# Performance work log

Hardware: AMD Instinct MI355X
Metric: run time of the kernel (lower is better)

The kernel has to match this reference:

```python
import jax, jax.numpy as jnp
import numpy as np

L, M, K, N = 131072, 511, 512, 512
STRIDE = (L - N) // (M - 1)  # 256; stride*(M-1)+N == L
B = 128
KH = K // 2 + 1  # 257 one-sided bins


def _tukey(n_pts, alpha=0.25):
    # scipy.signal.windows.tukey, sym=True
    n = np.arange(n_pts, dtype=np.float64)
    edge = alpha * (n_pts - 1) / 2.0
    w = np.ones(n_pts)
    left = n < edge
    w[left] = 0.5 * (1.0 + np.cos(np.pi * (2.0 * n[left] / (alpha * (n_pts - 1)) - 1.0)))
    right = n > (n_pts - 1) - edge
    w[right] = 0.5 * (1.0 + np.cos(np.pi * (2.0 * n[right] / (alpha * (n_pts - 1)) - 2.0 / alpha + 1.0)))
    return w


def _make_consts():
    w = _tukey(N, 0.25)
    w = (w / w.sum()).astype(np.float32)
    # fourier_matrix[n, k] = exp(-2*pi*i/N)**(n*k), sliced to K//2+1 cols, * sqrt(N)
    nk = np.outer(np.arange(N, dtype=np.float64), np.arange(K, dtype=np.float64))
    sigma = np.exp(-2j * np.pi / N)
    fm = (sigma ** nk)[:, :KH] * np.sqrt(N)
    return jnp.asarray(w), jnp.asarray(fm.astype(np.complex64))


def setup_inputs() -> dict:
    key = jax.random.key(0)
    x = jax.random.normal(key, (B, L), dtype=jnp.float32)
    window, fourier_matrix = _make_consts()
    return {"x": x, "window": window, "fourier_matrix": fourier_matrix}


def reference(x, window, fourier_matrix):
    xc = x.astype(jnp.complex64)
    xc = xc - jnp.mean(xc, axis=1, keepdims=True)
    # unfold(1, N, STRIDE) -> [B, M, N] overlapping frames
    idx = jnp.arange(M)[:, None] * STRIDE + jnp.arange(N)[None, :]  # [M, N]
    frames = xc[:, idx] * window[None, None, :].astype(jnp.complex64)  # [B, M, N]
    spec = jnp.matmul(frames, fourier_matrix)  # [B, M, KH] complex
    return jnp.abs(spec)
```

## Files before the change

kernel.cpp:

```cpp
#include <hip/hip_runtime.h>
#include <math.h>

#define L_LEN    131072
#define M_FRAMES 511
#define N_FFT    512
#define KH       257
#define FSTRIDE  256
#define B_BATCH  128

#define TM       32
#define RSTRIDE  36
#define SQRT_N   22.62741699796952f

typedef float pkf2 __attribute__((ext_vector_type(2)));

__device__ __forceinline__ pkf2 pk_fma(pkf2 a, pkf2 b, pkf2 c) {
    pkf2 d; asm("v_pk_fma_f32 %0, %1, %2, %3" : "=v"(d) : "v"(a), "v"(b), "v"(c)); return d;
}
__device__ __forceinline__ pkf2 pk_mul(pkf2 a, pkf2 b) {
    pkf2 d; asm("v_pk_mul_f32 %0, %1, %2" : "=v"(d) : "v"(a), "v"(b)); return d;
}
__device__ __forceinline__ float hw_sin_rev(float rev){float r;asm("v_sin_f32 %0, %1":"=v"(r):"v"(rev));return r;}
__device__ __forceinline__ float hw_cos_rev(float rev){float r;asm("v_cos_f32 %0, %1":"=v"(r):"v"(rev));return r;}

__global__ __launch_bounds__(256) void pmean_kernel(const float* __restrict__ x,
                                                    float* __restrict__ partial) {
    const int b = blockIdx.x >> 3, chunk = blockIdx.x & 7;
    const float4* p = (const float4*)(x + (size_t)b * L_LEN + (size_t)chunk * (L_LEN / 8));
    float s = 0.f;
    const int nvec = L_LEN / 8 / 4;
    for (int i = threadIdx.x; i < nvec; i += 256) {
        float4 v = p[i];
        s += (v.x + v.y) + (v.z + v.w);
    }
    for (int off = 32; off; off >>= 1) s += __shfl_down(s, off, 64);
    __shared__ float ws[4];
    if ((threadIdx.x & 63) == 0) ws[threadIdx.x >> 6] = s;
    __syncthreads();
    if (threadIdx.x == 0) partial[blockIdx.x] = (ws[0] + ws[1]) + (ws[2] + ws[3]);
}

__global__ __launch_bounds__(256, 2) void spec_kernel(const float* __restrict__ x,
                                                      const float* __restrict__ w,
                                                      const float* __restrict__ partial,
                                                      float* __restrict__ out) {
    __shared__ __align__(16) float lds[256 * RSTRIDE * 2 + 512 + 256];
    float* Es  = lds;
    float* Os  = lds + 256 * RSTRIDE;
    float* wl  = lds + 512 * RSTRIDE;
    float* nyq = wl + 512;

    const int b  = blockIdx.x;
    const int m0 = blockIdx.y * TM;
    const int t  = threadIdx.x;

    float msum = 0.f;
    #pragma unroll
    for (int i = 0; i < 8; ++i) msum += partial[(b << 3) + i];
    const float mean = msum * (1.0f / (float)L_LEN);

    wl[t]       = w[t];
    wl[t + 256] = w[t + 256];
    __syncthreads();

    {
        const int n = t;
        const float* xb = x + (size_t)b * L_LEN + (size_t)m0 * FSTRIDE;
        for (int f = 0; f < TM; ++f) {
            float Ev = 0.f, Ov = 0.f;
            if (m0 + f < M_FRAMES) {
                const float* xf = xb + f * FSTRIDE;
                if (n == 0) {
                    Ev = SQRT_N * ((xf[0]   - mean) * wl[0]);
                    Ov = SQRT_N * ((xf[256] - mean) * wl[256]);
                } else {
                    float a = (xf[n]       - mean) * wl[n];
                    float c = (xf[512 - n] - mean) * wl[512 - n];
                    Ev = SQRT_N * (a + c);
                    Ov = SQRT_N * (a - c);
                }
            }
            Es[n * RSTRIDE + f] = Ev;
            Os[n * RSTRIDE + f] = Ov;
        }
    }
    __syncthreads();

    const int kg = t & 63;
    const int fg = t >> 6;
    const float* Er = Es + 8 * fg;
    const float* Or = Os + 8 * fg;

    pkf2 re2[4][4], im2[4][4];

    {
        const float sg = (kg & 1) ? -1.f : 1.f;
        pkf2 sg2 = {sg, sg};
        #pragma unroll
        for (int j = 0; j < 4; ++j) {
            pkf2 e0 = *(const pkf2*)(Er + 2 * j);
            pkf2 o0 = *(const pkf2*)(Or + 2 * j);
            pkf2 r0 = pk_fma(sg2, o0, e0);
            #pragma unroll
            for (int u = 0; u < 4; ++u) { re2[u][j] = r0; im2[u][j] = (pkf2){0.f, 0.f}; }
        }
    }

    pkf2 ck2[4], sk2[4], msk2[4];
    #pragma unroll
    for (int u = 0; u < 4; ++u) {
        float rev = (float)(kg + 64 * u) * (1.0f / 512.0f);
        float ck = hw_cos_rev(rev), sk = hw_sin_rev(rev);
        ck2[u]  = (pkf2){ck, ck};
        sk2[u]  = (pkf2){sk, sk};
        msk2[u] = (pkf2){-sk, -sk};
    }

    #pragma unroll 1
    for (int seg = 0; seg < 4; ++seg) {
        const int n0   = seg ? seg * 64 : 1;
        const int nend = seg * 64 + 64;
        pkf2 c2[4], s2[4];
        #pragma unroll
        for (int u = 0; u < 4; ++u) {
            int p = (n0 * (kg + 64 * u)) & 511;
            float rev = (float)p * (1.0f / 512.0f);
            float c = hw_cos_rev(rev), s = hw_sin_rev(rev);
            c2[u] = (pkf2){c, c};
            s2[u] = (pkf2){s, s};
        }
        #pragma unroll 2
        for (int n = n0; n < nend; ++n) {
            const float* ern = Er + n * RSTRIDE;
            const float* orn = Or + n * RSTRIDE;
            pkf2 e2[4], o2[4];
            #pragma unroll
            for (int j = 0; j < 4; ++j) {
                e2[j] = *(const pkf2*)(ern + 2 * j);
                o2[j] = *(const pkf2*)(orn + 2 * j);
            }
            #pragma unroll
            for (int u = 0; u < 4; ++u) {
                re2[u][0] = pk_fma(e2[0], c2[u], re2[u][0]);
                im2[u][0] = pk_fma(o2[0], s2[u], im2[u][0]);
                re2[u][1] = pk_fma(e2[1], c2[u], re2[u][1]);
                im2[u][1] = pk_fma(o2[1], s2[u], im2[u][1]);
                re2[u][2] = pk_fma(e2[2], c2[u], re2[u][2]);
                im2[u][2] = pk_fma(o2[2], s2[u], im2[u][2]);
                re2[u][3] = pk_fma(e2[3], c2[u], re2[u][3]);
                im2[u][3] = pk_fma(o2[3], s2[u], im2[u][3]);
                pkf2 ta = pk_mul(c2[u], ck2[u]);
                pkf2 tb = pk_mul(c2[u], sk2[u]);
                c2[u] = pk_fma(s2[u], msk2[u], ta);
                s2[u] = pk_fma(s2[u], ck2[u],  tb);
            }
        }
    }

    #pragma unroll
    for (int u = 0; u < 4; ++u) {
        #pragma unroll
        for (int j = 0; j < 4; ++j) {
            const int f0 = fg * 8 + 2 * j;
            if (m0 + f0 < M_FRAMES) {
                float r = re2[u][j].x, ii = im2[u][j].x;
                out[((size_t)b * M_FRAMES + (m0 + f0)) * KH + kg + 64 * u] =
                    sqrtf(fmaf(r, r, ii * ii));
            }
            if (m0 + f0 + 1 < M_FRAMES) {
                float r = re2[u][j].y, ii = im2[u][j].y;
                out[((size_t)b * M_FRAMES + (m0 + f0 + 1)) * KH + kg + 64 * u] =
                    sqrtf(fmaf(r, r, ii * ii));
            }
        }
    }

    {
        const int g = t >> 5, f = t & 31;
        float acc = 0.f;
        const int nlo = g * 32;
        for (int n2 = nlo; n2 < nlo + 32; n2 += 2) {
            acc += Es[n2 * RSTRIDE + f] - Es[(n2 + 1) * RSTRIDE + f];
        }
        nyq[g * 32 + f] = acc;
    }
    __syncthreads();
    if (t < 32) {
        const int f = t;
        if (m0 + f < M_FRAMES) {
            float acc = Os[f];
            #pragma unroll
            for (int g = 0; g < 8; ++g) acc += nyq[g * 32 + f];
            out[((size_t)b * M_FRAMES + (m0 + f)) * KH + 256] = fabsf(acc);
        }
    }
}

extern "C" void kernel_launch(void* const* d_in, const int* in_sizes, int n_in,
                              void* d_out, int out_size, void* d_ws, size_t ws_size,
                              hipStream_t stream) {
    const float* x = (const float*)d_in[0];
    const float* w = (const float*)d_in[1];
    float* out     = (float*)d_out;
    float* partial = (float*)d_ws;

    pmean_kernel<<<dim3(B_BATCH * 8), dim3(256), 0, stream>>>(x, partial);

    const int mtiles = (M_FRAMES + TM - 1) / TM;
    spec_kernel<<<dim3(B_BATCH, mtiles), dim3(256), 0, stream>>>(x, w, partial, out);
}
```

Before: 370.4 us.

## Halve frame tile to 16 and raise occupancy to 4 blocks per CU

Shrinks the frame tile from 32 to 16, which halves the per-thread accumulator set (4 frames instead of 8) and the LDS footprint. Launch bounds now ask for 4 waves-per-EU worth of blocks. The n-loop is restructured into unrolled 4-step chunks through a helper, and the Nyquist scratch reuses the window buffer behind an extra barrier. The aim is more concurrent waves to hide LDS latency, at the cost of twice as many blocks and duplicated frame loads and twiddle recurrences per output.

```diff
diff --git a/kernel.cpp b/kernel.cpp
--- a/kernel.cpp
+++ b/kernel.cpp
@@ -8,8 +8,9 @@
 #define FSTRIDE  256
 #define B_BATCH  128
 
-#define TM       32
-#define RSTRIDE  36
+#define TM       16
+#define RSTRIDE  18
+#define OS_OFF   (256 * RSTRIDE)
 #define SQRT_N   22.62741699796952f
 
 typedef float pkf2 __attribute__((ext_vector_type(2)));
@@ -40,15 +41,37 @@
     if (threadIdx.x == 0) partial[blockIdx.x] = (ws[0] + ws[1]) + (ws[2] + ws[3]);
 }
 
-__global__ __launch_bounds__(256, 2) void spec_kernel(const float* __restrict__ x,
+__device__ __forceinline__ void nstep(const float* row,
+                                      pkf2 re2[4][2], pkf2 im2[4][2],
+                                      pkf2 c2[4], pkf2 s2[4],
+                                      const pkf2 ck2[4], const pkf2 sk2[4],
+                                      const pkf2 msk2[4]) {
+    pkf2 e0 = *(const pkf2*)(row);
+    pkf2 e1 = *(const pkf2*)(row + 2);
+    pkf2 o0 = *(const pkf2*)(row + OS_OFF);
+    pkf2 o1 = *(const pkf2*)(row + OS_OFF + 2);
+    #pragma unroll
+    for (int u = 0; u < 4; ++u) {
+        re2[u][0] = pk_fma(e0, c2[u], re2[u][0]);
+        im2[u][0] = pk_fma(o0, s2[u], im2[u][0]);
+        re2[u][1] = pk_fma(e1, c2[u], re2[u][1]);
+        im2[u][1] = pk_fma(o1, s2[u], im2[u][1]);
+        pkf2 ta = pk_mul(c2[u], ck2[u]);
+        pkf2 tb = pk_mul(c2[u], sk2[u]);
+        c2[u] = pk_fma(s2[u], msk2[u], ta);
+        s2[u] = pk_fma(s2[u], ck2[u],  tb);
+    }
+}
+
+__global__ __launch_bounds__(256, 4) void spec_kernel(const float* __restrict__ x,
                                                       const float* __restrict__ w,
                                                       const float* __restrict__ partial,
                                                       float* __restrict__ out) {
-    __shared__ __align__(16) float lds[256 * RSTRIDE * 2 + 512 + 256];
+    __shared__ __align__(16) float lds[512 * RSTRIDE + 512];
     float* Es  = lds;
-    float* Os  = lds + 256 * RSTRIDE;
+    float* Os  = lds + OS_OFF;
     float* wl  = lds + 512 * RSTRIDE;
-    float* nyq = wl + 512;
+    float* nyq = wl;
 
     const int b  = blockIdx.x;
     const int m0 = blockIdx.y * TM;
@@ -66,6 +89,7 @@
     {
         const int n = t;
         const float* xb = x + (size_t)b * L_LEN + (size_t)m0 * FSTRIDE;
+        #pragma unroll
         for (int f = 0; f < TM; ++f) {
             float Ev = 0.f, Ov = 0.f;
             if (m0 + f < M_FRAMES) {
@@ -88,21 +112,23 @@
 
     const int kg = t & 63;
     const int fg = t >> 6;
-    const float* Er = Es + 8 * fg;
-    const float* Or = Os + 8 * fg;
-
-    pkf2 re2[4][4], im2[4][4];
+    const float* Er = Es + 4 * fg;
+
+    pkf2 re2[4][2], im2[4][2];
 
     {
         const float sg = (kg & 1) ? -1.f : 1.f;
         pkf2 sg2 = {sg, sg};
-        #pragma unroll
-        for (int j = 0; j < 4; ++j) {
-            pkf2 e0 = *(const pkf2*)(Er + 2 * j);
-            pkf2 o0 = *(const pkf2*)(Or + 2 * j);
-            pkf2 r0 = pk_fma(sg2, o0, e0);
-            #pragma unroll
-            for (int u = 0; u < 4; ++u) { re2[u][j] = r0; im2[u][j] = (pkf2){0.f, 0.f}; }
+        pkf2 e0 = *(const pkf2*)(Er);
+        pkf2 e1 = *(const pkf2*)(Er + 2);
+        pkf2 o0 = *(const pkf2*)(Er + OS_OFF);
+        pkf2 o1 = *(const pkf2*)(Er + OS_OFF + 2);
+        pkf2 r0 = pk_fma(sg2, o0, e0);
+        pkf2 r1 = pk_fma(sg2, o1, e1);
+        #pragma unroll
+        for (int u = 0; u < 4; ++u) {
+            re2[u][0] = r0; re2[u][1] = r1;
+            im2[u][0] = (pkf2){0.f, 0.f}; im2[u][1] = (pkf2){0.f, 0.f};
         }
     }
 
@@ -118,8 +144,7 @@
 
     #pragma unroll 1
     for (int seg = 0; seg < 4; ++seg) {
-        const int n0   = seg ? seg * 64 : 1;
-        const int nend = seg * 64 + 64;
+        const int n0 = seg ? seg * 64 : 1;
         pkf2 c2[4], s2[4];
         #pragma unroll
         for (int u = 0; u < 4; ++u) {
@@ -129,39 +154,33 @@
             c2[u] = (pkf2){c, c};
             s2[u] = (pkf2){s, s};
         }
-        #pragma unroll 2
-        for (int n = n0; n < nend; ++n) {
-            const float* ern = Er + n * RSTRIDE;
-            const float* orn = Or + n * RSTRIDE;
-            pkf2 e2[4], o2[4];
-            #pragma unroll
-            for (int j = 0; j < 4; ++j) {
-                e2[j] = *(const pkf2*)(ern + 2 * j);
-                o2[j] = *(const pkf2*)(orn + 2 * j);
-            }
-            #pragma unroll
-            for (int u = 0; u < 4; ++u) {
-                re2[u][0] = pk_fma(e2[0], c2[u], re2[u][0]);
-                im2[u][0] = pk_fma(o2[0], s2[u], im2[u][0]);
-                re2[u][1] = pk_fma(e2[1], c2[u], re2[u][1]);
-                im2[u][1] = pk_fma(o2[1], s2[u], im2[u][1]);
-                re2[u][2] = pk_fma(e2[2], c2[u], re2[u][2]);
-                im2[u][2] = pk_fma(o2[2], s2[u], im2[u][2]);
-                re2[u][3] = pk_fma(e2[3], c2[u], re2[u][3]);
-                im2[u][3] = pk_fma(o2[3], s2[u], im2[u][3]);
-                pkf2 ta = pk_mul(c2[u], ck2[u]);
-                pkf2 tb = pk_mul(c2[u], sk2[u]);
-                c2[u] = pk_fma(s2[u], msk2[u], ta);
-                s2[u] = pk_fma(s2[u], ck2[u],  tb);
-            }
+        const float* pn;
+        int nch;
+        if (seg == 0) {
+            nstep(Er + 1 * RSTRIDE, re2, im2, c2, s2, ck2, sk2, msk2);
+            nstep(Er + 2 * RSTRIDE, re2, im2, c2, s2, ck2, sk2, msk2);
+            nstep(Er + 3 * RSTRIDE, re2, im2, c2, s2, ck2, sk2, msk2);
+            pn = Er + 4 * RSTRIDE;
+            nch = 15;
+        } else {
+            pn = Er + n0 * RSTRIDE;
+            nch = 16;
+        }
+        #pragma unroll 1
+        for (int ch = 0; ch < nch; ++ch) {
+            nstep(pn + 0 * RSTRIDE, re2, im2, c2, s2, ck2, sk2, msk2);
+            nstep(pn + 1 * RSTRIDE, re2, im2, c2, s2, ck2, sk2, msk2);
+            nstep(pn + 2 * RSTRIDE, re2, im2, c2, s2, ck2, sk2, msk2);
+            nstep(pn + 3 * RSTRIDE, re2, im2, c2, s2, ck2, sk2, msk2);
+            pn += 4 * RSTRIDE;
         }
     }
 
     #pragma unroll
     for (int u = 0; u < 4; ++u) {
         #pragma unroll
-        for (int j = 0; j < 4; ++j) {
-            const int f0 = fg * 8 + 2 * j;
+        for (int j = 0; j < 2; ++j) {
+            const int f0 = fg * 4 + 2 * j;
             if (m0 + f0 < M_FRAMES) {
                 float r = re2[u][j].x, ii = im2[u][j].x;
                 out[((size_t)b * M_FRAMES + (m0 + f0)) * KH + kg + 64 * u] =
@@ -176,21 +195,23 @@
     }
 
     {
-        const int g = t >> 5, f = t & 31;
+        const int g = t >> 4, f = t & 15;
         float acc = 0.f;
-        const int nlo = g * 32;
-        for (int n2 = nlo; n2 < nlo + 32; n2 += 2) {
-            acc += Es[n2 * RSTRIDE + f] - Es[(n2 + 1) * RSTRIDE + f];
-        }
-        nyq[g * 32 + f] = acc;
-    }
-    __syncthreads();
-    if (t < 32) {
+        const int nlo = g * 16;
+        #pragma unroll
+        for (int n2 = 0; n2 < 16; n2 += 2) {
+            acc += Es[(nlo + n2) * RSTRIDE + f] - Es[(nlo + n2 + 1) * RSTRIDE + f];
+        }
+        __syncthreads();
+        nyq[g * 16 + f] = acc;
+    }
+    __syncthreads();
+    if (t < TM) {
         const int f = t;
         if (m0 + f < M_FRAMES) {
             float acc = Os[f];
             #pragma unroll
-            for (int g = 0; g < 8; ++g) acc += nyq[g * 32 + f];
+            for (int g = 0; g < 16; ++g) acc += nyq[g * 16 + f];
             out[((size_t)b * M_FRAMES + (m0 + f)) * KH + 256] = fabsf(acc);
         }
     }
```

Result: slower. 423.6 us (+14.4%).
